# Performance work log

Measured on AMD Instinct MI355X. Metric: run time of the kernel, lower is better.

The kernel has to match this reference:

```python
import jax, jax.numpy as jnp
import numpy as np

PATCH = 9
EMBED = 768

def setup_inputs() -> dict:
    key = jax.random.key(0)
    k1, k2, k3, k4, k5, k6 = jax.random.split(key, 6)
    B, T, C, H, W = 4, 16, 3, 256, 256
    N = 8192
    patch_dim = PATCH * PATCH * C  # 243
    frames = jax.random.normal(k1, (B, T, C, H, W), dtype=jnp.float32)
    coords = jax.random.uniform(k2, (B, N, 2), dtype=jnp.float32)
    t_src = jax.random.randint(k3, (B, N), 0, T, dtype=jnp.int32)
    # MLP params (Linear: y = x @ W + b), kaiming-ish scale
    W1 = jax.random.normal(k4, (patch_dim, EMBED), dtype=jnp.float32) / np.sqrt(patch_dim)
    b1 = jnp.zeros((EMBED,), dtype=jnp.float32)
    W2 = jax.random.normal(k5, (EMBED, EMBED), dtype=jnp.float32) / np.sqrt(EMBED)
    b2 = jnp.zeros((EMBED,), dtype=jnp.float32)
    return {"frames": frames, "coords": coords, "t_src": t_src,
            "W1": W1, "b1": b1, "W2": W2, "b2": b2}

def reference(frames, coords, t_src, W1, b1, W2, b2):
    B, T, C, H, W = frames.shape
    N = coords.shape[1]
    half = PATCH // 2
    # integer center pixel (coords in [0,1] -> truncation == floor for nonneg)
    u = (coords[..., 0] * (W - 1)).astype(jnp.int32)  # (B, N)
    v = (coords[..., 1] * (H - 1)).astype(jnp.int32)
    off = jnp.arange(PATCH, dtype=jnp.int32) - half    # (P,)
    # replicate padding at borders == clamped gather indices
    ys = jnp.clip(v[..., None] + off, 0, H - 1)        # (B, N, P)
    xs = jnp.clip(u[..., None] + off, 0, W - 1)        # (B, N, P)
    fp = jnp.transpose(frames, (0, 1, 3, 4, 2))        # (B, T, H, W, C)
    bidx = jnp.arange(B, dtype=jnp.int32)[:, None, None, None]
    # gather patches: (B, N, P, P, C)
    patches = fp[bidx, t_src[:, :, None, None].astype(jnp.int32),
                 ys[:, :, :, None], xs[:, :, None, :]]
    x = patches.reshape(B, N, PATCH * PATCH * C)       # (B, N, 243)
    h = jax.nn.gelu(x @ W1 + b1, approximate=False)    # torch nn.GELU = exact erf
    return h @ W2 + b2                                 # (B, N, EMBED)
```

## Files before the change

kernel.cpp:

```cpp
#include <hip/hip_runtime.h>
#include <math.h>


typedef __attribute__((ext_vector_type(8))) short short8;
typedef __attribute__((ext_vector_type(4))) float floatx4;

#define M_ROWS 32768
#define KPAD   256
#define EMB    768

typedef __attribute__((address_space(1))) const void g_void;
typedef __attribute__((address_space(3))) void l_void;

__device__ __forceinline__ unsigned short f2bf(float f) {
    union { float f; unsigned int i; } w;
    w.f = f;
    unsigned int x = w.i;
    x += 0x7fffu + ((x >> 16) & 1u);
    return (unsigned short)(x >> 16);
}

__device__ __forceinline__ float gelu_f(float x) {
    float x3 = x * x * x;
    float y  = 1.5957691216f * (x + 0.044715f * x3);
    float e  = __expf(y);
    float th = 1.0f - 2.0f / (e + 1.0f);
    return 0.5f * x * (1.0f + th);
}

__global__ void k_transpose_w1(const float* __restrict__ W1,
                               unsigned short* __restrict__ W1T) {
    int idx = blockIdx.x * 256 + threadIdx.x;
    int n  = idx >> 8;
    int kp = idx & 255;
    unsigned short v = 0;
    if (kp < 243) {
        int c = kp / 81;
        int r = kp - c * 81;
        int i = r / 9;
        int j = r - i * 9;
        int e = i * 27 + j * 3 + c;
        v = f2bf(W1[e * EMB + n]);
    }
    W1T[idx] = v;
}

__global__ void k_transpose_w2(const float* __restrict__ W2,
                               unsigned short* __restrict__ W2T) {
    __shared__ float tile[32][33];
    int tx = threadIdx.x & 31, ty = threadIdx.x >> 5;
    int k0 = blockIdx.x * 32, n0 = blockIdx.y * 32;
#pragma unroll
    for (int i = 0; i < 4; ++i)
        tile[ty + i * 8][tx] = W2[(size_t)(k0 + ty + i * 8) * EMB + n0 + tx];
    __syncthreads();
#pragma unroll
    for (int i = 0; i < 4; ++i)
        W2T[(size_t)(n0 + ty + i * 8) * EMB + k0 + tx] = f2bf(tile[tx][ty + i * 8]);
}

__global__ void k_gather(const float* __restrict__ frames,
                         const float* __restrict__ coords,
                         const int* __restrict__ t_src,
                         unsigned short* __restrict__ X) {
    int row  = blockIdx.x * 4 + (threadIdx.x >> 6);
    int lane = threadIdx.x & 63;
    int b = row >> 13;

    float cu = coords[row * 2 + 0];
    float cv = coords[row * 2 + 1];
    int u = (int)(cu * 255.0f);
    int v = (int)(cv * 255.0f);
    int t = t_src[row];

    const float* fb = frames + (size_t)(b * 16 + t) * (3 * 256 * 256);
    unsigned short* xr = X + (size_t)row * KPAD;

#pragma unroll
    for (int it = 0; it < 4; ++it) {
        int kp = lane + it * 64;
        unsigned short val = 0;
        if (kp < 243) {
            int c = kp / 81;
            int r = kp - c * 81;
            int i = r / 9;
            int j = r - i * 9;
            int y = v + i - 4; y = (y < 0) ? 0 : (y > 255 ? 255 : y);
            int x = u + j - 4; x = (x < 0) ? 0 : (x > 255 ? 255 : x);
            val = f2bf(fb[(size_t)c * 65536 + y * 256 + x]);
        }
        xr[kp] = val;
    }
}

template <int K, bool GELU, bool OUT_F32>
__device__ __forceinline__
void gemm_body(const unsigned short* __restrict__ A,
               const unsigned short* __restrict__ BT,
               const float* __restrict__ bias,
               void* __restrict__ Cv) {
    __shared__ unsigned short As[2][128 * 64];
    __shared__ unsigned short Bs[2][128 * 64];

    int tid  = threadIdx.x;
    int wave = tid >> 6;
    int lane = tid & 63;
    int wm = (wave >> 1) * 64;
    int wn = (wave & 1) * 64;
    int lm = lane & 15;
    int lq = lane >> 4;

    int m0 = blockIdx.x * 128;
    int n0 = blockIdx.y * 128;

    floatx4 acc[4][4];
#pragma unroll
    for (int i = 0; i < 4; ++i)
#pragma unroll
        for (int j = 0; j < 4; ++j)
            acc[i][j] = (floatx4){0.f, 0.f, 0.f, 0.f};

    const unsigned short* Ag = A  + (size_t)m0 * K;
    const unsigned short* Bg = BT + (size_t)n0 * K;

    int rl    = lane >> 3;
    int pslot = lane & 7;

#pragma unroll
    for (int i = 0; i < 4; ++i) {
        int chunk = wave * 4 + i;
        int r     = chunk * 8 + rl;
        int lslot = pslot ^ (r & 7);
        __builtin_amdgcn_global_load_lds((g_void*)(Ag + (size_t)r * K + (lslot << 3)),
                                         (l_void*)(&As[0][chunk * 512]), 16, 0, 0);
        __builtin_amdgcn_global_load_lds((g_void*)(Bg + (size_t)r * K + (lslot << 3)),
                                         (l_void*)(&Bs[0][chunk * 512]), 16, 0, 0);
    }

    int buf = 0;
    for (int k0 = 0; k0 < K; k0 += 64) {
        __syncthreads();

        if (k0 + 64 < K) {
#pragma unroll
            for (int i = 0; i < 4; ++i) {
                int chunk = wave * 4 + i;
                int r     = chunk * 8 + rl;
                int lslot = pslot ^ (r & 7);
                __builtin_amdgcn_global_load_lds(
                    (g_void*)(Ag + (size_t)r * K + k0 + 64 + (lslot << 3)),
                    (l_void*)(&As[buf ^ 1][chunk * 512]), 16, 0, 0);
                __builtin_amdgcn_global_load_lds(
                    (g_void*)(Bg + (size_t)r * K + k0 + 64 + (lslot << 3)),
                    (l_void*)(&Bs[buf ^ 1][chunk * 512]), 16, 0, 0);
            }
        }

#pragma unroll
        for (int ks = 0; ks < 2; ++ks) {
            short8 af[4], bfr[4];
#pragma unroll
            for (int mi = 0; mi < 4; ++mi) {
                int row = wm + mi * 16 + lm;
                int ps  = ((ks << 2) + lq) ^ (row & 7);
                af[mi] = *(const short8*)(&As[buf][row * 64 + (ps << 3)]);
            }
#pragma unroll
            for (int ni = 0; ni < 4; ++ni) {
                int row = wn + ni * 16 + lm;
                int ps  = ((ks << 2) + lq) ^ (row & 7);
                bfr[ni] = *(const short8*)(&Bs[buf][row * 64 + (ps << 3)]);
            }
#pragma unroll
            for (int mi = 0; mi < 4; ++mi)
#pragma unroll
                for (int ni = 0; ni < 4; ++ni)
                    acc[mi][ni] = __builtin_amdgcn_mfma_f32_16x16x32_bf16(
                        af[mi], bfr[ni], acc[mi][ni], 0, 0, 0);
        }
        buf ^= 1;
    }

#pragma unroll
    for (int ni = 0; ni < 4; ++ni) {
        int col = n0 + wn + ni * 16 + lm;
        float bs = bias[col];
#pragma unroll
        for (int mi = 0; mi < 4; ++mi) {
            int rowb = m0 + wm + mi * 16 + lq * 4;
#pragma unroll
            for (int r = 0; r < 4; ++r) {
                float x = acc[mi][ni][r] + bs;
                if (GELU)
                    x = gelu_f(x);
                size_t idx = (size_t)(rowb + r) * EMB + col;
                if (OUT_F32)
                    ((float*)Cv)[idx] = x;
                else
                    ((unsigned short*)Cv)[idx] = f2bf(x);
            }
        }
    }
}

__global__ __launch_bounds__(256, 2)
void k_gemm1(const unsigned short* __restrict__ A, const unsigned short* __restrict__ BT,
             const float* __restrict__ bias, unsigned short* __restrict__ C) {
    gemm_body<KPAD, true, false>(A, BT, bias, (void*)C);
}

__global__ __launch_bounds__(256, 2)
void k_gemm2(const unsigned short* __restrict__ A, const unsigned short* __restrict__ BT,
             const float* __restrict__ bias, float* __restrict__ C) {
    gemm_body<EMB, false, true>(A, BT, bias, (void*)C);
}

extern "C" void kernel_launch(void* const* d_in, const int* in_sizes, int n_in,
                              void* d_out, int out_size, void* d_ws, size_t ws_size,
                              hipStream_t stream) {
    const float* frames = (const float*)d_in[0];
    const float* coords = (const float*)d_in[1];
    const int*   t_src  = (const int*)d_in[2];
    const float* W1     = (const float*)d_in[3];
    const float* b1     = (const float*)d_in[4];
    const float* W2     = (const float*)d_in[5];
    const float* b2     = (const float*)d_in[6];
    float* out = (float*)d_out;

    char* ws = (char*)d_ws;
    unsigned short* X    = (unsigned short*)(ws);
    unsigned short* Hbuf = (unsigned short*)(ws + 16777216);
    unsigned short* W1T  = (unsigned short*)(ws + 16777216 + 50331648);
    unsigned short* W2T  = (unsigned short*)(ws + 16777216 + 50331648 + 393216);

    k_transpose_w1<<<768, 256, 0, stream>>>(W1, W1T);
    k_transpose_w2<<<dim3(24, 24), 256, 0, stream>>>(W2, W2T);

    k_gather<<<M_ROWS / 4, 256, 0, stream>>>(frames, coords, t_src, X);

    k_gemm1<<<dim3(M_ROWS / 128, EMB / 128), 256, 0, stream>>>(X, W1T, b1, Hbuf);

    k_gemm2<<<dim3(M_ROWS / 128, EMB / 128), 256, 0, stream>>>(Hbuf, W2T, b2, out);
}
```

Measured before the change: 243.5 us.

## Rewrite GEMMs as 256x256 tiles with 8 waves and phased ping-pong pipeline

Replaces the 128x128, 4-wave GEMM with a 256x256 tile computed by 8 waves (512 threads). The K loop is split into explicit phases that interleave LDS fragment reads, async global-to-LDS staging and MFMA quadrants, using hand-placed barriers, waitcnt checkpoints and setprio. The goal is more data reuse per tile and more overlap of memory with matrix work. In exchange the tile uses 128 KB of LDS and 128 accumulator registers per thread, which limits occupancy, and the grid shrinks to 384 blocks, which may leave CUs poorly balanced.

```diff
diff --git a/kernel.cpp b/kernel.cpp
--- a/kernel.cpp
+++ b/kernel.cpp
@@ -93,107 +93,189 @@
     }
 }
 
-template <int K, bool GELU, bool OUT_F32>
-__device__ __forceinline__
-void gemm_body(const unsigned short* __restrict__ A,
-               const unsigned short* __restrict__ BT,
-               const float* __restrict__ bias,
-               void* __restrict__ Cv) {
-    __shared__ unsigned short As[2][128 * 64];
-    __shared__ unsigned short Bs[2][128 * 64];
-
-    int tid  = threadIdx.x;
-    int wave = tid >> 6;
-    int lane = tid & 63;
-    int wm = (wave >> 1) * 64;
-    int wn = (wave & 1) * 64;
-    int lm = lane & 15;
-    int lq = lane >> 4;
-
-    int m0 = blockIdx.x * 128;
-    int n0 = blockIdx.y * 128;
-
-    floatx4 acc[4][4];
-#pragma unroll
-    for (int i = 0; i < 4; ++i)
+
+#define STAGE_A(B_, H_, KT_) do {                                              \
+    __builtin_amdgcn_global_load_lds(                                          \
+        (g_void*)(Ag + oS##H_##0 + (size_t)(KT_) * 64),                        \
+        (l_void*)(&As[B_][H_][c0 * 512]), 16, 0, 0);                           \
+    __builtin_amdgcn_global_load_lds(                                          \
+        (g_void*)(Ag + oS##H_##1 + (size_t)(KT_) * 64),                        \
+        (l_void*)(&As[B_][H_][c1 * 512]), 16, 0, 0);                           \
+} while (0)
+
+#define STAGE_B(B_, H_, KT_) do {                                              \
+    __builtin_amdgcn_global_load_lds(                                          \
+        (g_void*)(Bg + oS##H_##0 + (size_t)(KT_) * 64),                        \
+        (l_void*)(&Bs[B_][H_][c0 * 512]), 16, 0, 0);                           \
+    __builtin_amdgcn_global_load_lds(                                          \
+        (g_void*)(Bg + oS##H_##1 + (size_t)(KT_) * 64),                        \
+        (l_void*)(&Bs[B_][H_][c1 * 512]), 16, 0, 0);                           \
+} while (0)
+
+#define LDA(DST, B_, MH) do {                                                  \
+    _Pragma("unroll")                                                          \
+    for (int mi_ = 0; mi_ < 4; ++mi_) {                                        \
+        DST[0][mi_] = *(const short8*)&As[B_][wm][(MH)*4096 + mi_*1024 + aof0];\
+        DST[1][mi_] = *(const short8*)&As[B_][wm][(MH)*4096 + mi_*1024 + aof1];\
+    }                                                                          \
+} while (0)
+
+#define LDB(B_, NH) do {                                                       \
+    _Pragma("unroll")                                                          \
+    for (int ni_ = 0; ni_ < 2; ++ni_) {                                        \
+        bb[0][ni_] = *(const short8*)&Bs[B_][bh][bn64 + (NH)*2048 + ni_*1024 + aof0]; \
+        bb[1][ni_] = *(const short8*)&Bs[B_][bh][bn64 + (NH)*2048 + ni_*1024 + aof1]; \
+    }                                                                          \
+} while (0)
+
+#define MFMA_Q(MH, NH, ASET) do {                                              \
+    _Pragma("unroll")                                                          \
+    for (int ks_ = 0; ks_ < 2; ++ks_)                                          \
+    { _Pragma("unroll")                                                        \
+      for (int mi_ = 0; mi_ < 4; ++mi_)                                        \
+      { _Pragma("unroll")                                                      \
+        for (int ni_ = 0; ni_ < 2; ++ni_)                                      \
+            acc[(MH)*4 + mi_][(NH)*2 + ni_] =                                  \
+                __builtin_amdgcn_mfma_f32_16x16x32_bf16(                       \
+                    ASET[ks_][mi_], bb[ks_][ni_],                              \
+                    acc[(MH)*4 + mi_][(NH)*2 + ni_], 0, 0, 0);                 \
+      } }                                                                      \
+} while (0)
+
+#define SYNC_MFMA(MH, NH, ASET) do {                                           \
+    __builtin_amdgcn_s_barrier();                                              \
+    asm volatile("s_waitcnt lgkmcnt(0)" ::: "memory");                         \
+    __builtin_amdgcn_sched_barrier(0);                                         \
+    __builtin_amdgcn_s_setprio(1);                                             \
+    MFMA_Q(MH, NH, ASET);                                                      \
+    __builtin_amdgcn_s_setprio(0);                                             \
+} while (0)
+
+#define END_PHASE do {                                                         \
+    __builtin_amdgcn_s_barrier();                                              \
+    __builtin_amdgcn_sched_barrier(0);                                         \
+} while (0)
+
+#define CKPT(N_) do {                                                          \
+    asm volatile("s_waitcnt vmcnt(" #N_ ")" ::: "memory");                     \
+    __builtin_amdgcn_s_barrier();                                              \
+    __builtin_amdgcn_sched_barrier(0);                                         \
+} while (0)
+
+#define ITER_STEADY(T0) do {                                                   \
+     LDA(a0, 0, 0); LDB(0, 0); STAGE_B(1, 0, (T0)+1);                  \
+             SYNC_MFMA(0, 0, a0); END_PHASE;                                   \
+     LDA(a1, 0, 1); STAGE_B(1, 1, (T0)+1);                             \
+             SYNC_MFMA(1, 0, a1); END_PHASE;                                   \
+     LDB(0, 1); STAGE_A(0, 0, (T0)+2);                                 \
+             SYNC_MFMA(0, 1, a0); END_PHASE;                                   \
+     STAGE_A(0, 1, (T0)+2);                                            \
+             SYNC_MFMA(1, 1, a1); CKPT(4);                                     \
+     LDA(a0, 1, 0); LDB(1, 0); STAGE_B(0, 0, (T0)+2);                  \
+             SYNC_MFMA(0, 0, a0); END_PHASE;                                   \
+     LDA(a1, 1, 1); STAGE_B(0, 1, (T0)+2);                             \
+             SYNC_MFMA(1, 0, a1); END_PHASE;                                   \
+     LDB(1, 1); STAGE_A(1, 0, (T0)+3);                                 \
+             SYNC_MFMA(0, 1, a0); END_PHASE;                                   \
+     STAGE_A(1, 1, (T0)+3);                                            \
+             SYNC_MFMA(1, 1, a1); CKPT(4);                                     \
+} while (0)
+
+#define ITER_FINAL(T0) do {                                                    \
+     LDA(a0, 0, 0); LDB(0, 0); STAGE_B(1, 0, (T0)+1);                  \
+             SYNC_MFMA(0, 0, a0); END_PHASE;                                   \
+     LDA(a1, 0, 1); STAGE_B(1, 1, (T0)+1);                             \
+             SYNC_MFMA(1, 0, a1); END_PHASE;                                   \
+     LDB(0, 1);                                                        \
+             SYNC_MFMA(0, 1, a0); END_PHASE;                                   \
+     SYNC_MFMA(1, 1, a1); CKPT(0);                                     \
+     LDA(a0, 1, 0); LDB(1, 0);                                         \
+             SYNC_MFMA(0, 0, a0); END_PHASE;                                   \
+     LDA(a1, 1, 1);                                                    \
+             SYNC_MFMA(1, 0, a1); END_PHASE;                                   \
+     LDB(1, 1);                                                        \
+             SYNC_MFMA(0, 1, a0); END_PHASE;                                   \
+     SYNC_MFMA(1, 1, a1);                                              \
+} while (0)
+
+template <int K, bool GELU_, bool OUT_F32>
+static __device__ __forceinline__
+void gemm8_body(const unsigned short* __restrict__ A,
+                const unsigned short* __restrict__ BT,
+                const float* __restrict__ bias,
+                void* __restrict__ Cv) {
+    constexpr int KT  = K / 64;
+    constexpr int NIT = KT / 2;
+    static_assert(KT >= 4 && (KT & 1) == 0, "K must be multiple of 128, >=256");
+
+    __shared__ unsigned short As[2][2][128 * 64];
+    __shared__ unsigned short Bs[2][2][128 * 64];
+
+    const int tid  = threadIdx.x;
+    const int wave = tid >> 6;
+    const int lane = tid & 63;
+    const int wm = wave >> 2;
+    const int wn = wave & 3;
+    const int bh = wn >> 1;
+    const int bn64 = (wn & 1) * 4096;
+    const int lm = lane & 15;
+    const int lq = lane >> 4;
+
+    const int m0 = blockIdx.x * 256;
+    const int n0 = blockIdx.y * 256;
+
+    const int aof0 = lm * 64 + (((0 << 2) + lq) ^ (lm & 7)) * 8;
+    const int aof1 = lm * 64 + (((1 << 2) + lq) ^ (lm & 7)) * 8;
+
+    const int rl = lane >> 3;
+    const int pl = lane & 7;
+    const int c0 = wave * 2, c1 = wave * 2 + 1;
+    const int r0 = c0 * 8 + rl, r1 = c1 * 8 + rl;
+    const size_t slog8 = (size_t)((pl ^ rl) * 8);
+    const size_t oS00 = (size_t)(r0)       * K + slog8;
+    const size_t oS01 = (size_t)(r1)       * K + slog8;
+    const size_t oS10 = (size_t)(128 + r0) * K + slog8;
+    const size_t oS11 = (size_t)(128 + r1) * K + slog8;
+
+    const unsigned short* Ag = A  + (size_t)m0 * K;
+    const unsigned short* Bg = BT + (size_t)n0 * K;
+
+    floatx4 acc[8][4];
+#pragma unroll
+    for (int i = 0; i < 8; ++i)
 #pragma unroll
         for (int j = 0; j < 4; ++j)
             acc[i][j] = (floatx4){0.f, 0.f, 0.f, 0.f};
 
-    const unsigned short* Ag = A  + (size_t)m0 * K;
-    const unsigned short* Bg = BT + (size_t)n0 * K;
-
-    int rl    = lane >> 3;
-    int pslot = lane & 7;
-
-#pragma unroll
-    for (int i = 0; i < 4; ++i) {
-        int chunk = wave * 4 + i;
-        int r     = chunk * 8 + rl;
-        int lslot = pslot ^ (r & 7);
-        __builtin_amdgcn_global_load_lds((g_void*)(Ag + (size_t)r * K + (lslot << 3)),
-                                         (l_void*)(&As[0][chunk * 512]), 16, 0, 0);
-        __builtin_amdgcn_global_load_lds((g_void*)(Bg + (size_t)r * K + (lslot << 3)),
-                                         (l_void*)(&Bs[0][chunk * 512]), 16, 0, 0);
+    short8 a0[2][4], a1[2][4], bb[2][2];
+
+    STAGE_A(0, 0, 0); STAGE_A(0, 1, 0);
+    STAGE_B(0, 0, 0); STAGE_B(0, 1, 0);
+    STAGE_A(1, 0, 1); STAGE_A(1, 1, 1);
+    asm volatile("s_waitcnt vmcnt(4)" ::: "memory");
+    __builtin_amdgcn_s_barrier();
+    __builtin_amdgcn_sched_barrier(0);
+
+#pragma unroll 1
+    for (int it = 0; it < NIT - 1; ++it) {
+        const int t0 = 2 * it;
+        ITER_STEADY(t0);
     }
-
-    int buf = 0;
-    for (int k0 = 0; k0 < K; k0 += 64) {
-        __syncthreads();
-
-        if (k0 + 64 < K) {
-#pragma unroll
-            for (int i = 0; i < 4; ++i) {
-                int chunk = wave * 4 + i;
-                int r     = chunk * 8 + rl;
-                int lslot = pslot ^ (r & 7);
-                __builtin_amdgcn_global_load_lds(
-                    (g_void*)(Ag + (size_t)r * K + k0 + 64 + (lslot << 3)),
-                    (l_void*)(&As[buf ^ 1][chunk * 512]), 16, 0, 0);
-                __builtin_amdgcn_global_load_lds(
-                    (g_void*)(Bg + (size_t)r * K + k0 + 64 + (lslot << 3)),
-                    (l_void*)(&Bs[buf ^ 1][chunk * 512]), 16, 0, 0);
-            }
-        }
-
-#pragma unroll
-        for (int ks = 0; ks < 2; ++ks) {
-            short8 af[4], bfr[4];
-#pragma unroll
-            for (int mi = 0; mi < 4; ++mi) {
-                int row = wm + mi * 16 + lm;
-                int ps  = ((ks << 2) + lq) ^ (row & 7);
-                af[mi] = *(const short8*)(&As[buf][row * 64 + (ps << 3)]);
-            }
-#pragma unroll
-            for (int ni = 0; ni < 4; ++ni) {
-                int row = wn + ni * 16 + lm;
-                int ps  = ((ks << 2) + lq) ^ (row & 7);
-                bfr[ni] = *(const short8*)(&Bs[buf][row * 64 + (ps << 3)]);
-            }
-#pragma unroll
-            for (int mi = 0; mi < 4; ++mi)
-#pragma unroll
-                for (int ni = 0; ni < 4; ++ni)
-                    acc[mi][ni] = __builtin_amdgcn_mfma_f32_16x16x32_bf16(
-                        af[mi], bfr[ni], acc[mi][ni], 0, 0, 0);
-        }
-        buf ^= 1;
-    }
-
-#pragma unroll
-    for (int ni = 0; ni < 4; ++ni) {
-        int col = n0 + wn + ni * 16 + lm;
-        float bs = bias[col];
-#pragma unroll
-        for (int mi = 0; mi < 4; ++mi) {
-            int rowb = m0 + wm + mi * 16 + lq * 4;
-#pragma unroll
-            for (int r = 0; r < 4; ++r) {
-                float x = acc[mi][ni][r] + bs;
-                if (GELU)
+    ITER_FINAL(2 * (NIT - 1));
+
+#pragma unroll
+    for (int ng = 0; ng < 4; ++ng) {
+        const int col = n0 + wn * 64 + ng * 16 + lm;
+        const float bs = bias[col];
+#pragma unroll
+        for (int mg = 0; mg < 8; ++mg) {
+            const int rowb = m0 + wm * 128 + mg * 16 + lq * 4;
+#pragma unroll
+            for (int r2 = 0; r2 < 4; ++r2) {
+                float x = acc[mg][ng][r2] + bs;
+                if (GELU_)
                     x = gelu_f(x);
-                size_t idx = (size_t)(rowb + r) * EMB + col;
+                size_t idx = (size_t)(rowb + r2) * EMB + col;
                 if (OUT_F32)
                     ((float*)Cv)[idx] = x;
                 else
@@ -203,16 +285,16 @@
     }
 }
 
-__global__ __launch_bounds__(256, 2)
+__global__ __launch_bounds__(512, 2)
 void k_gemm1(const unsigned short* __restrict__ A, const unsigned short* __restrict__ BT,
              const float* __restrict__ bias, unsigned short* __restrict__ C) {
-    gemm_body<KPAD, true, false>(A, BT, bias, (void*)C);
-}
-
-__global__ __launch_bounds__(256, 2)
+    gemm8_body<KPAD, true, false>(A, BT, bias, (void*)C);
+}
+
+__global__ __launch_bounds__(512, 2)
 void k_gemm2(const unsigned short* __restrict__ A, const unsigned short* __restrict__ BT,
              const float* __restrict__ bias, float* __restrict__ C) {
-    gemm_body<EMB, false, true>(A, BT, bias, (void*)C);
+    gemm8_body<EMB, false, true>(A, BT, bias, (void*)C);
 }
 
 extern "C" void kernel_launch(void* const* d_in, const int* in_sizes, int n_in,
@@ -238,7 +320,7 @@
 
     k_gather<<<M_ROWS / 4, 256, 0, stream>>>(frames, coords, t_src, X);
 
-    k_gemm1<<<dim3(M_ROWS / 128, EMB / 128), 256, 0, stream>>>(X, W1T, b1, Hbuf);
-
-    k_gemm2<<<dim3(M_ROWS / 128, EMB / 128), 256, 0, stream>>>(Hbuf, W2T, b2, out);
-}
+    k_gemm1<<<dim3(M_ROWS / 256, EMB / 256), 512, 0, stream>>>(X, W1T, b1, Hbuf);
+
+    k_gemm2<<<dim3(M_ROWS / 256, EMB / 256), 512, 0, stream>>>(Hbuf, W2T, b2, out);
+}
```

New measurement: 268.0 us. 1.1x slower.

## Use 8-wave GEMM blocks with swizzled 1D grid for L2 reuse

Applied to the files above, without the earlier changes.

Both GEMM kernels now launch 512 threads (8 waves, 2x4 layout, each wave owning a 64x32 output sub-tile) instead of 4 waves with 64x64 sub-tiles. This halves per-wave accumulator registers and adds more waves to hide latency, and the global-to-LDS loads are redistributed so each wave issues two chunks per operand. The 2D grid is replaced by a 1D grid remapped through an XCD-style swizzle, so neighbouring M tiles sharing the same weight columns land on the same chiplet and reuse L2. The trade-off is more LDS reads per MFMA, since each wave re-reads A fragments for a narrower N slice, and the launch bound now asks for four 512-thread blocks per CU.

```diff
diff --git a/kernel.cpp b/kernel.cpp
--- a/kernel.cpp
+++ b/kernel.cpp
@@ -93,8 +93,8 @@
     }
 }
 
-template <int K, bool GELU, bool OUT_F32>
-__device__ __forceinline__
+template <int K, bool GELU_, bool OUT_F32>
+static __device__ __forceinline__
 void gemm_body(const unsigned short* __restrict__ A,
                const unsigned short* __restrict__ BT,
                const float* __restrict__ bias,
@@ -102,79 +102,78 @@
     __shared__ unsigned short As[2][128 * 64];
     __shared__ unsigned short Bs[2][128 * 64];
 
-    int tid  = threadIdx.x;
-    int wave = tid >> 6;
-    int lane = tid & 63;
-    int wm = (wave >> 1) * 64;
-    int wn = (wave & 1) * 64;
-    int lm = lane & 15;
-    int lq = lane >> 4;
-
-    int m0 = blockIdx.x * 128;
-    int n0 = blockIdx.y * 128;
-
-    floatx4 acc[4][4];
+    const int tid  = threadIdx.x;
+    const int wave = tid >> 6;
+    const int lane = tid & 63;
+    const int wr = wave >> 2;
+    const int wc = wave & 3;
+    const int lm = lane & 15;
+    const int lq = lane >> 4;
+
+    const int bid = blockIdx.x;
+    const int swz = (bid & 7) * 192 + (bid >> 3);
+    const int by  = swz % 6;
+    const int bx  = swz / 6;
+    const int m0 = bx * 128;
+    const int n0 = by * 128;
+
+    floatx4 acc[4][2];
 #pragma unroll
     for (int i = 0; i < 4; ++i)
 #pragma unroll
-        for (int j = 0; j < 4; ++j)
+        for (int j = 0; j < 2; ++j)
             acc[i][j] = (floatx4){0.f, 0.f, 0.f, 0.f};
 
     const unsigned short* Ag = A  + (size_t)m0 * K;
     const unsigned short* Bg = BT + (size_t)n0 * K;
 
-    int rl    = lane >> 3;
-    int pslot = lane & 7;
-
-#pragma unroll
-    for (int i = 0; i < 4; ++i) {
-        int chunk = wave * 4 + i;
-        int r     = chunk * 8 + rl;
-        int lslot = pslot ^ (r & 7);
-        __builtin_amdgcn_global_load_lds((g_void*)(Ag + (size_t)r * K + (lslot << 3)),
-                                         (l_void*)(&As[0][chunk * 512]), 16, 0, 0);
-        __builtin_amdgcn_global_load_lds((g_void*)(Bg + (size_t)r * K + (lslot << 3)),
-                                         (l_void*)(&Bs[0][chunk * 512]), 16, 0, 0);
-    }
+    const int rl    = lane >> 3;
+    const int pl    = lane & 7;
+    const int lslot = pl ^ rl;
+    const int c0 = wave;
+    const int c1 = 8 + wave;
+    const size_t o0 = (size_t)(c0 * 8 + rl) * K + (lslot << 3);
+    const size_t o1 = (size_t)(c1 * 8 + rl) * K + (lslot << 3);
+
+    __builtin_amdgcn_global_load_lds((g_void*)(Ag + o0), (l_void*)(&As[0][c0 * 512]), 16, 0, 0);
+    __builtin_amdgcn_global_load_lds((g_void*)(Ag + o1), (l_void*)(&As[0][c1 * 512]), 16, 0, 0);
+    __builtin_amdgcn_global_load_lds((g_void*)(Bg + o0), (l_void*)(&Bs[0][c0 * 512]), 16, 0, 0);
+    __builtin_amdgcn_global_load_lds((g_void*)(Bg + o1), (l_void*)(&Bs[0][c1 * 512]), 16, 0, 0);
 
     int buf = 0;
     for (int k0 = 0; k0 < K; k0 += 64) {
         __syncthreads();
 
         if (k0 + 64 < K) {
-#pragma unroll
-            for (int i = 0; i < 4; ++i) {
-                int chunk = wave * 4 + i;
-                int r     = chunk * 8 + rl;
-                int lslot = pslot ^ (r & 7);
-                __builtin_amdgcn_global_load_lds(
-                    (g_void*)(Ag + (size_t)r * K + k0 + 64 + (lslot << 3)),
-                    (l_void*)(&As[buf ^ 1][chunk * 512]), 16, 0, 0);
-                __builtin_amdgcn_global_load_lds(
-                    (g_void*)(Bg + (size_t)r * K + k0 + 64 + (lslot << 3)),
-                    (l_void*)(&Bs[buf ^ 1][chunk * 512]), 16, 0, 0);
-            }
+            __builtin_amdgcn_global_load_lds((g_void*)(Ag + o0 + k0 + 64),
+                                             (l_void*)(&As[buf ^ 1][c0 * 512]), 16, 0, 0);
+            __builtin_amdgcn_global_load_lds((g_void*)(Ag + o1 + k0 + 64),
+                                             (l_void*)(&As[buf ^ 1][c1 * 512]), 16, 0, 0);
+            __builtin_amdgcn_global_load_lds((g_void*)(Bg + o0 + k0 + 64),
+                                             (l_void*)(&Bs[buf ^ 1][c0 * 512]), 16, 0, 0);
+            __builtin_amdgcn_global_load_lds((g_void*)(Bg + o1 + k0 + 64),
+                                             (l_void*)(&Bs[buf ^ 1][c1 * 512]), 16, 0, 0);
         }
 
 #pragma unroll
         for (int ks = 0; ks < 2; ++ks) {
-            short8 af[4], bfr[4];
+            short8 af[4], bfr[2];
 #pragma unroll
             for (int mi = 0; mi < 4; ++mi) {
-                int row = wm + mi * 16 + lm;
+                int row = wr * 64 + mi * 16 + lm;
                 int ps  = ((ks << 2) + lq) ^ (row & 7);
                 af[mi] = *(const short8*)(&As[buf][row * 64 + (ps << 3)]);
             }
 #pragma unroll
-            for (int ni = 0; ni < 4; ++ni) {
-                int row = wn + ni * 16 + lm;
+            for (int ni = 0; ni < 2; ++ni) {
+                int row = wc * 32 + ni * 16 + lm;
                 int ps  = ((ks << 2) + lq) ^ (row & 7);
                 bfr[ni] = *(const short8*)(&Bs[buf][row * 64 + (ps << 3)]);
             }
 #pragma unroll
             for (int mi = 0; mi < 4; ++mi)
 #pragma unroll
-                for (int ni = 0; ni < 4; ++ni)
+                for (int ni = 0; ni < 2; ++ni)
                     acc[mi][ni] = __builtin_amdgcn_mfma_f32_16x16x32_bf16(
                         af[mi], bfr[ni], acc[mi][ni], 0, 0, 0);
         }
@@ -182,16 +181,16 @@
     }
 
 #pragma unroll
-    for (int ni = 0; ni < 4; ++ni) {
-        int col = n0 + wn + ni * 16 + lm;
+    for (int ni = 0; ni < 2; ++ni) {
+        int col = n0 + wc * 32 + ni * 16 + lm;
         float bs = bias[col];
 #pragma unroll
         for (int mi = 0; mi < 4; ++mi) {
-            int rowb = m0 + wm + mi * 16 + lq * 4;
+            int rowb = m0 + wr * 64 + mi * 16 + lq * 4;
 #pragma unroll
             for (int r = 0; r < 4; ++r) {
                 float x = acc[mi][ni][r] + bs;
-                if (GELU)
+                if (GELU_)
                     x = gelu_f(x);
                 size_t idx = (size_t)(rowb + r) * EMB + col;
                 if (OUT_F32)
@@ -203,13 +202,13 @@
     }
 }
 
-__global__ __launch_bounds__(256, 2)
+__global__ __launch_bounds__(512, 4)
 void k_gemm1(const unsigned short* __restrict__ A, const unsigned short* __restrict__ BT,
              const float* __restrict__ bias, unsigned short* __restrict__ C) {
     gemm_body<KPAD, true, false>(A, BT, bias, (void*)C);
 }
 
-__global__ __launch_bounds__(256, 2)
+__global__ __launch_bounds__(512, 4)
 void k_gemm2(const unsigned short* __restrict__ A, const unsigned short* __restrict__ BT,
              const float* __restrict__ bias, float* __restrict__ C) {
     gemm_body<EMB, false, true>(A, BT, bias, (void*)C);
@@ -238,7 +237,7 @@
 
     k_gather<<<M_ROWS / 4, 256, 0, stream>>>(frames, coords, t_src, X);
 
-    k_gemm1<<<dim3(M_ROWS / 128, EMB / 128), 256, 0, stream>>>(X, W1T, b1, Hbuf);
-
-    k_gemm2<<<dim3(M_ROWS / 128, EMB / 128), 256, 0, stream>>>(Hbuf, W2T, b2, out);
-}
+    k_gemm1<<<1536, 512, 0, stream>>>(X, W1T, b1, Hbuf);
+
+    k_gemm2<<<1536, 512, 0, stream>>>(Hbuf, W2T, b2, out);
+}
```

Measured after the change: 228.7 us. -6.1%, faster.
